# Performance work log

Measured on AMD Instinct MI355X. Metric: run time of the kernel, lower is better.

Reference implementation:

```python
import jax, jax.numpy as jnp
import numpy as np

BIG = 1e10


def _cylinder_query(radius, hmin, hmax, nsample, xyz, new_xyz, rot):
    # xyz: (B,N,3), new_xyz: (B,P,3), rot: (B,P,3,3) -> idx: (B,P,nsample) int32
    diff = xyz[:, None, :, :] - new_xyz[:, :, None, :]          # (B,P,N,3)
    local = jnp.einsum('bpnc,bpcd->bpnd', diff, rot)            # (B,P,N,3)
    x, y, z = local[..., 0], local[..., 1], local[..., 2]
    r2 = y * y + z * z                                          # (B,P,N)
    in_cyl = (x >= hmin) & (x <= hmax) & (r2 < radius * radius)
    dist = jnp.where(in_cyl, r2, BIG)
    neg_vals, idx = jax.lax.top_k(-dist, nsample)               # smallest dists
    vals = -neg_vals
    valid = vals < 1e9
    first = idx[:, :, 0:1]
    idx = jnp.where(valid, idx, first)                          # (B,P,nsample)
    return idx


def _group(features, idx):
    # features: (B,C,N), idx: (B,P,S) -> (B,C,P,S)
    B, C, N = features.shape
    P, S = idx.shape[1], idx.shape[2]
    ft = jnp.swapaxes(features, 1, 2)                           # (B,N,C)
    flat = idx.reshape(B, P * S)
    out = jnp.take_along_axis(ft, flat[:, :, None], axis=1)     # (B,P*S,C)
    return jnp.transpose(out.reshape(B, P, S, C), (0, 3, 1, 2)) # (B,C,P,S)


def setup_inputs() -> dict:
    key = jax.random.key(0)
    k1, k2, k3, k4 = jax.random.split(key, 4)
    B, N, P, C = 4, 16384, 1024, 64
    xyz = jax.random.uniform(k1, (B, N, 3), dtype=jnp.float32)
    new_xyz = jax.random.uniform(k2, (B, P, 3), dtype=jnp.float32)
    rot = jax.random.normal(k3, (B, P, 3, 3), dtype=jnp.float32)
    features = jax.random.normal(k4, (B, C, N), dtype=jnp.float32)
    return {"radius": 0.3, "hmin": -0.02, "hmax": 0.04, "nsample": 32,
            "xyz": xyz, "new_xyz": new_xyz, "rot": rot, "features": features}


def reference(radius, hmin, hmax, nsample, xyz, new_xyz, rot, features):
    idx = _cylinder_query(radius, hmin, hmax, nsample, xyz, new_xyz, rot)
    xyz_t = jnp.swapaxes(xyz, 1, 2)                             # (B,3,N)
    grouped_xyz = _group(xyz_t, idx)                            # (B,3,P,S)
    grouped_xyz = grouped_xyz - jnp.swapaxes(new_xyz, 1, 2)[..., None]
    # rotate_xyz=True: (B,P,S,3) @ (B,P,3,3)
    g = jnp.transpose(grouped_xyz, (0, 2, 3, 1))
    g = jnp.einsum('bpsc,bpcd->bpsd', g, rot)
    grouped_xyz = jnp.transpose(g, (0, 3, 1, 2))                # (B,3,P,S)
    grouped_features = _group(features, idx)                    # (B,C,P,S)
    return jnp.concatenate([grouped_xyz, grouped_features], axis=1)
```

## Files before the change

kernel.cpp:

```cpp
#include <hip/hip_runtime.h>

#define CAP    4608
#define BIGK   1.0e300
#define IDXINF 0x7fffffff

__device__ __forceinline__ void cmpx(double& k, int& n, int lane, int stride, bool up) {
    double ok = __shfl_xor(k, stride);
    int    on = __shfl_xor(n, stride);
    bool oLess = (ok < k) || (ok == k && on < n);
    bool lower = (lane & stride) == 0;
    bool takeOther = lower ? (up ? oLess : !oLess) : (up ? !oLess : oLess);
    if (takeOther) { k = ok; n = on; }
}

__device__ __forceinline__ void wave_sort64(double& k, int& n, int lane, bool asc) {
    #pragma unroll
    for (int size = 2; size < 64; size <<= 1) {
        bool up = asc ? ((lane & size) == 0) : ((lane & size) != 0);
        #pragma unroll
        for (int stride = size >> 1; stride > 0; stride >>= 1)
            cmpx(k, n, lane, stride, up);
    }
    #pragma unroll
    for (int stride = 32; stride > 0; stride >>= 1)
        cmpx(k, n, lane, stride, asc);
}

__global__ __launch_bounds__(256, 8) void select_kernel(
    const float* __restrict__ radius_p,
    const float* __restrict__ hmin_p,
    const float* __restrict__ hmax_p,
    const float* __restrict__ xyz,
    const float* __restrict__ new_xyz,
    const float* __restrict__ rot,
    float* __restrict__ out,
    unsigned short* __restrict__ selw)
{
    const int N = 16384, P = 1024, S = 32, OC = 67;
    const int bp  = blockIdx.x;
    const int b   = bp >> 10;
    const int p   = bp & (P - 1);
    const int tid = threadIdx.x;
    const int lane = tid & 63;
    const int wv   = tid >> 6;

    __shared__ unsigned short cn[CAP];
    __shared__ double wr2[256];
    __shared__ int    wn[256];
    __shared__ int    cnt;
    __shared__ int    cnt2;
    __shared__ int    sel[32];

    if (tid == 0) { cnt = 0; cnt2 = 0; }
    __syncthreads();

    const double radius = (double)radius_p[0];
    const double hmin   = (double)hmin_p[0];
    const double hmax   = (double)hmax_p[0];
    const double rad2   = radius * radius;

    const float* nx = new_xyz + (size_t)bp * 3;
    const double cx = nx[0], cy = nx[1], cz = nx[2];
    const float* rp = rot + (size_t)bp * 9;
    const double r00 = rp[0], r01 = rp[1], r02 = rp[2];
    const double r10 = rp[3], r11 = rp[4], r12 = rp[5];
    const double r20 = rp[6], r21 = rp[7], r22 = rp[8];

    const float r00f = (float)r00, r01f = (float)r01, r02f = (float)r02;
    const float r10f = (float)r10, r11f = (float)r11, r12f = (float)r12;
    const float r20f = (float)r20, r21f = (float)r21, r22f = (float)r22;
    const float cpxf = (float)(cx * r00 + cy * r10 + cz * r20);
    const float cpyf = (float)(cx * r01 + cy * r11 + cz * r21);
    const float cpzf = (float)(cx * r02 + cy * r12 + cz * r22);
    const float hminf = (float)hmin - 5.0e-4f;
    const float hmaxf = (float)hmax + 5.0e-4f;
    const float rad2f = (float)rad2 + 1.0e-3f;

    const float* xb = xyz + (size_t)b * N * 3;
    const float4* vp = reinterpret_cast<const float4*>(xb);

    float4 a0 = vp[tid * 3 + 0], a1 = vp[tid * 3 + 1], a2 = vp[tid * 3 + 2];
    for (int it = 0; it < 16; ++it) {
        const float4* q = vp + ((it + 1) & 15) * 768 + tid * 3;
        float4 b0 = q[0], b1 = q[1], b2 = q[2];
        int g = it * 1024 + tid * 4;
        float px[4], py[4], pz[4];
        px[0]=a0.x; py[0]=a0.y; pz[0]=a0.z;
        px[1]=a0.w; py[1]=a1.x; pz[1]=a1.y;
        px[2]=a1.z; py[2]=a1.w; pz[2]=a2.x;
        px[3]=a2.y; py[3]=a2.z; pz[3]=a2.w;
        #pragma unroll
        for (int k = 0; k < 4; ++k) {
            float xf  = fmaf(px[k], r00f, fmaf(py[k], r10f, fmaf(pz[k], r20f, -cpxf)));
            float yf  = fmaf(px[k], r01f, fmaf(py[k], r11f, fmaf(pz[k], r21f, -cpyf)));
            float zf  = fmaf(px[k], r02f, fmaf(py[k], r12f, fmaf(pz[k], r22f, -cpzf)));
            float r2f = fmaf(yf, yf, zf * zf);
            if (xf >= hminf && xf <= hmaxf && r2f < rad2f) {
                int slot = atomicAdd(&cnt, 1);
                if (slot < CAP) cn[slot] = (unsigned short)(g + k);
            }
        }
        a0 = b0; a1 = b1; a2 = b2;
    }
    __syncthreads();

    int  Mloose = cnt;
    bool ident  = false;
    if (Mloose > CAP) { Mloose = N; ident = true; }

    double rk = BIGK; int rn = IDXINF;
    int msum = 0;
    const int nch = (Mloose + 63) >> 6;
    for (int ch = wv; ch < nch; ch += 4) {
        int j = (ch << 6) + lane;
        double ck = BIGK; int cnn = IDXINF;
        bool ok = false;
        if (j < Mloose) {
            int n = ident ? j : (int)cn[j];
            double dx = (double)xb[n * 3 + 0] - cx;
            double dy = (double)xb[n * 3 + 1] - cy;
            double dz = (double)xb[n * 3 + 2] - cz;
            double x = dx * r00 + dy * r10 + dz * r20;
            double y = dx * r01 + dy * r11 + dz * r21;
            double z = dx * r02 + dy * r12 + dz * r22;
            double r2 = y * y + z * z;
            if (x >= hmin && x <= hmax && r2 < rad2) { ok = true; ck = r2; cnn = n; }
        }
        msum += __popcll(__ballot(ok));
        wave_sort64(ck, cnn, lane, false);
        if ((ck < rk) || (ck == rk && cnn < rn)) { rk = ck; rn = cnn; }
        #pragma unroll
        for (int stride = 32; stride > 0; stride >>= 1)
            cmpx(rk, rn, lane, stride, true);
    }
    if (lane == 0 && msum > 0) atomicAdd(&cnt2, msum);
    wr2[(wv << 6) + lane] = rk;
    wn [(wv << 6) + lane] = rn;
    __syncthreads();

    if (wv == 0) {
        const int Mtrue = cnt2;
        #pragma unroll
        for (int w = 1; w < 4; ++w) {
            int src = (w << 6) + (63 - lane);
            double ck = wr2[src]; int cnn = wn[src];
            if ((ck < rk) || (ck == rk && cnn < rn)) { rk = ck; rn = cnn; }
            #pragma unroll
            for (int stride = 32; stride > 0; stride >>= 1)
                cmpx(rk, rn, lane, stride, true);
        }
        int nsel  = min(Mtrue, S);
        int first = __shfl(rn, 0);
        int v = (lane < nsel) ? rn : ((nsel > 0) ? first : 0);
        if (lane < S) sel[lane] = v;
    }
    __syncthreads();

    if (tid < S) {
        int n = sel[tid];
        selw[(size_t)bp * S + tid] = (unsigned short)n;
        double dx = (double)xb[n * 3 + 0] - cx;
        double dy = (double)xb[n * 3 + 1] - cy;
        double dz = (double)xb[n * 3 + 2] - cz;
        float x = (float)(dx * r00 + dy * r10 + dz * r20);
        float y = (float)(dx * r01 + dy * r11 + dz * r21);
        float z = (float)(dx * r02 + dy * r12 + dz * r22);
        float* o = out + (((size_t)b * OC + 0) * P + p) * S + tid;
        o[0 * (size_t)P * S] = x;
        o[1 * (size_t)P * S] = y;
        o[2 * (size_t)P * S] = z;
    }
}

__global__ __launch_bounds__(1024, 8) void gather_kernel(
    const float* __restrict__ feat,
    const unsigned short* __restrict__ selw,
    float* __restrict__ out)
{
    const int N = 16384, P = 1024, C = 64, S = 32, OC = 67;
    const int bid  = blockIdx.x;
    const int c    = bid & 63;
    const int half = (bid >> 6) & 1;
    const int b    = bid >> 7;
    const int tid  = threadIdx.x;

    __shared__ unsigned short st[512 * 32];

    const uint4* sp = reinterpret_cast<const uint4*>(
        selw + ((size_t)b * P + half * 512) * S);
    uint4* dl = reinterpret_cast<uint4*>(st);
    dl[tid]        = sp[tid];
    dl[1024 + tid] = sp[1024 + tid];
    __syncthreads();

    const float* fr = feat + ((size_t)b * C + c) * N;
    float* ob = out + (((size_t)b * OC + 3 + c) * P + half * 512) * S;

    int   ix[16];
    float v [16];
    #pragma unroll
    for (int k = 0; k < 16; ++k)
        ix[k] = st[k * 1024 + tid];
    #pragma unroll
    for (int k = 0; k < 16; ++k)
        v[k] = fr[ix[k]];
    #pragma unroll
    for (int k = 0; k < 16; ++k)
        __builtin_nontemporal_store(v[k], &ob[k * 1024 + tid]);
}

extern "C" void kernel_launch(void* const* d_in, const int* in_sizes, int n_in,
                              void* d_out, int out_size, void* d_ws, size_t ws_size,
                              hipStream_t stream) {
    const float* radius  = (const float*)d_in[0];
    const float* hmin    = (const float*)d_in[1];
    const float* hmax    = (const float*)d_in[2];
    const float* xyz     = (const float*)d_in[4];
    const float* new_xyz = (const float*)d_in[5];
    const float* rot     = (const float*)d_in[6];
    const float* feat    = (const float*)d_in[7];
    float* out = (float*)d_out;
    unsigned short* selw = (unsigned short*)d_ws;

    hipLaunchKernelGGL(select_kernel, dim3(4096), dim3(256), 0, stream,
                       radius, hmin, hmax, xyz, new_xyz, rot, out, selw);
    hipLaunchKernelGGL(gather_kernel, dim3(512), dim3(1024), 0, stream,
                       feat, selw, out);
}
```

Measured before the change: 108.7 us.

## Process four query points per block to reuse streamed point loads

Each select block now handles four query centers: one pass over the batch's points tests every point against all four cylinders, appending candidates to per-query shared lists. The refinement and sort stage then runs sequentially for each query. This is meant to cut the repeated global/L2 reads of the full point cloud by 4x and reduce block launch count. In exchange, it uses more registers, more shared memory, a lower occupancy target and fewer blocks, and it serializes the per-query selection inside a block.

```diff
diff --git a/kernel.cpp b/kernel.cpp
--- a/kernel.cpp
+++ b/kernel.cpp
@@ -1,6 +1,7 @@
 #include <hip/hip_runtime.h>
 
-#define CAP    4608
+#define QPB    4
+#define CAP    4544
 #define BIGK   1.0e300
 #define IDXINF 0x7fffffff
 
@@ -26,7 +27,7 @@
         cmpx(k, n, lane, stride, asc);
 }
 
-__global__ __launch_bounds__(256, 8) void select_kernel(
+__global__ __launch_bounds__(256, 4) void select_kernel(
     const float* __restrict__ radius_p,
     const float* __restrict__ hmin_p,
     const float* __restrict__ hmax_p,
@@ -37,52 +38,56 @@
     unsigned short* __restrict__ selw)
 {
     const int N = 16384, P = 1024, S = 32, OC = 67;
-    const int bp  = blockIdx.x;
-    const int b   = bp >> 10;
-    const int p   = bp & (P - 1);
+    const int bid = blockIdx.x;
+    const int b   = bid >> 8;
+    const int p0  = (bid & 255) * QPB;
     const int tid = threadIdx.x;
     const int lane = tid & 63;
     const int wv   = tid >> 6;
 
-    __shared__ unsigned short cn[CAP];
+    __shared__ unsigned short cn[QPB][CAP];
     __shared__ double wr2[256];
     __shared__ int    wn[256];
-    __shared__ int    cnt;
-    __shared__ int    cnt2;
+    __shared__ int    cnt[QPB];
+    __shared__ int    cnt2[QPB];
     __shared__ int    sel[32];
 
-    if (tid == 0) { cnt = 0; cnt2 = 0; }
+    if (tid < QPB) { cnt[tid] = 0; cnt2[tid] = 0; }
     __syncthreads();
 
-    const double radius = (double)radius_p[0];
-    const double hmin   = (double)hmin_p[0];
-    const double hmax   = (double)hmax_p[0];
-    const double rad2   = radius * radius;
-
-    const float* nx = new_xyz + (size_t)bp * 3;
-    const double cx = nx[0], cy = nx[1], cz = nx[2];
-    const float* rp = rot + (size_t)bp * 9;
-    const double r00 = rp[0], r01 = rp[1], r02 = rp[2];
-    const double r10 = rp[3], r11 = rp[4], r12 = rp[5];
-    const double r20 = rp[6], r21 = rp[7], r22 = rp[8];
-
-    const float r00f = (float)r00, r01f = (float)r01, r02f = (float)r02;
-    const float r10f = (float)r10, r11f = (float)r11, r12f = (float)r12;
-    const float r20f = (float)r20, r21f = (float)r21, r22f = (float)r22;
-    const float cpxf = (float)(cx * r00 + cy * r10 + cz * r20);
-    const float cpyf = (float)(cx * r01 + cy * r11 + cz * r21);
-    const float cpzf = (float)(cx * r02 + cy * r12 + cz * r22);
+    const double hmin = (double)hmin_p[0];
+    const double hmax = (double)hmax_p[0];
+    const double rad  = (double)radius_p[0];
+    const double rad2 = rad * rad;
     const float hminf = (float)hmin - 5.0e-4f;
     const float hmaxf = (float)hmax + 5.0e-4f;
     const float rad2f = (float)rad2 + 1.0e-3f;
 
+    float R00[QPB], R01[QPB], R02[QPB], R10[QPB], R11[QPB], R12[QPB],
+          R20[QPB], R21[QPB], R22[QPB], CPX[QPB], CPY[QPB], CPZ[QPB];
+    #pragma unroll
+    for (int q = 0; q < QPB; ++q) {
+        const float* rp = rot     + ((size_t)(b * P + p0 + q)) * 9;
+        const float* nx = new_xyz + ((size_t)(b * P + p0 + q)) * 3;
+        double r00 = rp[0], r01 = rp[1], r02 = rp[2];
+        double r10 = rp[3], r11 = rp[4], r12 = rp[5];
+        double r20 = rp[6], r21 = rp[7], r22 = rp[8];
+        double cx = nx[0], cy = nx[1], cz = nx[2];
+        R00[q] = (float)r00; R01[q] = (float)r01; R02[q] = (float)r02;
+        R10[q] = (float)r10; R11[q] = (float)r11; R12[q] = (float)r12;
+        R20[q] = (float)r20; R21[q] = (float)r21; R22[q] = (float)r22;
+        CPX[q] = (float)(cx * r00 + cy * r10 + cz * r20);
+        CPY[q] = (float)(cx * r01 + cy * r11 + cz * r21);
+        CPZ[q] = (float)(cx * r02 + cy * r12 + cz * r22);
+    }
+
     const float* xb = xyz + (size_t)b * N * 3;
     const float4* vp = reinterpret_cast<const float4*>(xb);
 
     float4 a0 = vp[tid * 3 + 0], a1 = vp[tid * 3 + 1], a2 = vp[tid * 3 + 2];
     for (int it = 0; it < 16; ++it) {
-        const float4* q = vp + ((it + 1) & 15) * 768 + tid * 3;
-        float4 b0 = q[0], b1 = q[1], b2 = q[2];
+        const float4* qv = vp + ((it + 1) & 15) * 768 + tid * 3;
+        float4 b0 = qv[0], b1 = qv[1], b2 = qv[2];
         int g = it * 1024 + tid * 4;
         float px[4], py[4], pz[4];
         px[0]=a0.x; py[0]=a0.y; pz[0]=a0.z;
@@ -91,84 +96,100 @@
         px[3]=a2.y; py[3]=a2.z; pz[3]=a2.w;
         #pragma unroll
         for (int k = 0; k < 4; ++k) {
-            float xf  = fmaf(px[k], r00f, fmaf(py[k], r10f, fmaf(pz[k], r20f, -cpxf)));
-            float yf  = fmaf(px[k], r01f, fmaf(py[k], r11f, fmaf(pz[k], r21f, -cpyf)));
-            float zf  = fmaf(px[k], r02f, fmaf(py[k], r12f, fmaf(pz[k], r22f, -cpzf)));
-            float r2f = fmaf(yf, yf, zf * zf);
-            if (xf >= hminf && xf <= hmaxf && r2f < rad2f) {
-                int slot = atomicAdd(&cnt, 1);
-                if (slot < CAP) cn[slot] = (unsigned short)(g + k);
+            #pragma unroll
+            for (int q = 0; q < QPB; ++q) {
+                float xf  = fmaf(px[k], R00[q], fmaf(py[k], R10[q], fmaf(pz[k], R20[q], -CPX[q])));
+                float yf  = fmaf(px[k], R01[q], fmaf(py[k], R11[q], fmaf(pz[k], R21[q], -CPY[q])));
+                float zf  = fmaf(px[k], R02[q], fmaf(py[k], R12[q], fmaf(pz[k], R22[q], -CPZ[q])));
+                float r2f = fmaf(yf, yf, zf * zf);
+                if (xf >= hminf && xf <= hmaxf && r2f < rad2f) {
+                    int slot = atomicAdd(&cnt[q], 1);
+                    if (slot < CAP) cn[q][slot] = (unsigned short)(g + k);
+                }
             }
         }
         a0 = b0; a1 = b1; a2 = b2;
     }
     __syncthreads();
 
-    int  Mloose = cnt;
-    bool ident  = false;
-    if (Mloose > CAP) { Mloose = N; ident = true; }
-
-    double rk = BIGK; int rn = IDXINF;
-    int msum = 0;
-    const int nch = (Mloose + 63) >> 6;
-    for (int ch = wv; ch < nch; ch += 4) {
-        int j = (ch << 6) + lane;
-        double ck = BIGK; int cnn = IDXINF;
-        bool ok = false;
-        if (j < Mloose) {
-            int n = ident ? j : (int)cn[j];
-            double dx = (double)xb[n * 3 + 0] - cx;
-            double dy = (double)xb[n * 3 + 1] - cy;
-            double dz = (double)xb[n * 3 + 2] - cz;
-            double x = dx * r00 + dy * r10 + dz * r20;
-            double y = dx * r01 + dy * r11 + dz * r21;
-            double z = dx * r02 + dy * r12 + dz * r22;
-            double r2 = y * y + z * z;
-            if (x >= hmin && x <= hmax && r2 < rad2) { ok = true; ck = r2; cnn = n; }
-        }
-        msum += __popcll(__ballot(ok));
-        wave_sort64(ck, cnn, lane, false);
-        if ((ck < rk) || (ck == rk && cnn < rn)) { rk = ck; rn = cnn; }
-        #pragma unroll
-        for (int stride = 32; stride > 0; stride >>= 1)
-            cmpx(rk, rn, lane, stride, true);
-    }
-    if (lane == 0 && msum > 0) atomicAdd(&cnt2, msum);
-    wr2[(wv << 6) + lane] = rk;
-    wn [(wv << 6) + lane] = rn;
-    __syncthreads();
-
-    if (wv == 0) {
-        const int Mtrue = cnt2;
-        #pragma unroll
-        for (int w = 1; w < 4; ++w) {
-            int src = (w << 6) + (63 - lane);
-            double ck = wr2[src]; int cnn = wn[src];
+    #pragma unroll 1
+    for (int q = 0; q < QPB; ++q) {
+        const int bp = b * P + p0 + q;
+        const int p  = p0 + q;
+        const float* rp = rot     + (size_t)bp * 9;
+        const float* nx = new_xyz + (size_t)bp * 3;
+        const double r00 = rp[0], r01 = rp[1], r02 = rp[2];
+        const double r10 = rp[3], r11 = rp[4], r12 = rp[5];
+        const double r20 = rp[6], r21 = rp[7], r22 = rp[8];
+        const double cx = nx[0], cy = nx[1], cz = nx[2];
+
+        int  Mloose = cnt[q];
+        bool ident  = false;
+        if (Mloose > CAP) { Mloose = N; ident = true; }
+
+        double rk = BIGK; int rn = IDXINF;
+        int msum = 0;
+        const int nch = (Mloose + 63) >> 6;
+        for (int ch = wv; ch < nch; ch += 4) {
+            int j = (ch << 6) + lane;
+            double ck = BIGK; int cnn = IDXINF;
+            bool ok = false;
+            if (j < Mloose) {
+                int n = ident ? j : (int)cn[q][j];
+                double dx = (double)xb[n * 3 + 0] - cx;
+                double dy = (double)xb[n * 3 + 1] - cy;
+                double dz = (double)xb[n * 3 + 2] - cz;
+                double x = dx * r00 + dy * r10 + dz * r20;
+                double y = dx * r01 + dy * r11 + dz * r21;
+                double z = dx * r02 + dy * r12 + dz * r22;
+                double r2 = y * y + z * z;
+                if (x >= hmin && x <= hmax && r2 < rad2) { ok = true; ck = r2; cnn = n; }
+            }
+            msum += __popcll(__ballot(ok));
+            wave_sort64(ck, cnn, lane, false);
             if ((ck < rk) || (ck == rk && cnn < rn)) { rk = ck; rn = cnn; }
             #pragma unroll
             for (int stride = 32; stride > 0; stride >>= 1)
                 cmpx(rk, rn, lane, stride, true);
         }
-        int nsel  = min(Mtrue, S);
-        int first = __shfl(rn, 0);
-        int v = (lane < nsel) ? rn : ((nsel > 0) ? first : 0);
-        if (lane < S) sel[lane] = v;
-    }
-    __syncthreads();
-
-    if (tid < S) {
-        int n = sel[tid];
-        selw[(size_t)bp * S + tid] = (unsigned short)n;
-        double dx = (double)xb[n * 3 + 0] - cx;
-        double dy = (double)xb[n * 3 + 1] - cy;
-        double dz = (double)xb[n * 3 + 2] - cz;
-        float x = (float)(dx * r00 + dy * r10 + dz * r20);
-        float y = (float)(dx * r01 + dy * r11 + dz * r21);
-        float z = (float)(dx * r02 + dy * r12 + dz * r22);
-        float* o = out + (((size_t)b * OC + 0) * P + p) * S + tid;
-        o[0 * (size_t)P * S] = x;
-        o[1 * (size_t)P * S] = y;
-        o[2 * (size_t)P * S] = z;
+        if (lane == 0 && msum > 0) atomicAdd(&cnt2[q], msum);
+        wr2[(wv << 6) + lane] = rk;
+        wn [(wv << 6) + lane] = rn;
+        __syncthreads();
+
+        if (wv == 0) {
+            const int Mtrue = cnt2[q];
+            #pragma unroll
+            for (int w = 1; w < 4; ++w) {
+                int src = (w << 6) + (63 - lane);
+                double ck = wr2[src]; int cnn = wn[src];
+                if ((ck < rk) || (ck == rk && cnn < rn)) { rk = ck; rn = cnn; }
+                #pragma unroll
+                for (int stride = 32; stride > 0; stride >>= 1)
+                    cmpx(rk, rn, lane, stride, true);
+            }
+            int nsel  = min(Mtrue, S);
+            int first = __shfl(rn, 0);
+            int v = (lane < nsel) ? rn : ((nsel > 0) ? first : 0);
+            if (lane < S) sel[lane] = v;
+        }
+        __syncthreads();
+
+        if (tid < S) {
+            int n = sel[tid];
+            selw[(size_t)bp * S + tid] = (unsigned short)n;
+            double dx = (double)xb[n * 3 + 0] - cx;
+            double dy = (double)xb[n * 3 + 1] - cy;
+            double dz = (double)xb[n * 3 + 2] - cz;
+            float x = (float)(dx * r00 + dy * r10 + dz * r20);
+            float y = (float)(dx * r01 + dy * r11 + dz * r21);
+            float z = (float)(dx * r02 + dy * r12 + dz * r22);
+            float* o = out + (((size_t)b * OC + 0) * P + p) * S + tid;
+            o[0 * (size_t)P * S] = x;
+            o[1 * (size_t)P * S] = y;
+            o[2 * (size_t)P * S] = z;
+        }
+        __syncthreads();
     }
 }
 
@@ -222,7 +243,7 @@
     float* out = (float*)d_out;
     unsigned short* selw = (unsigned short*)d_ws;
 
-    hipLaunchKernelGGL(select_kernel, dim3(4096), dim3(256), 0, stream,
+    hipLaunchKernelGGL(select_kernel, dim3(1024), dim3(256), 0, stream,
                        radius, hmin, hmax, xyz, new_xyz, rot, out, selw);
     hipLaunchKernelGGL(gather_kernel, dim3(512), dim3(1024), 0, stream,
                        feat, selw, out);
```

Result: slower. 131.3 us (+20.8%).
